# Optimization experiments

Measured on AMD Instinct MI355X. Metric: run time of the kernel, lower is better.

The kernel has to match this reference:

```python
import jax, jax.numpy as jnp
import numpy as np

B, A, H, W = 16, 3, 80, 80
NUM_CLASSES = 80
C = 4 + NUM_CLASSES  # box(4) + [obj-as-class0 + remaining classes]
N_TGT = 64


def setup_inputs() -> dict:
    key = jax.random.key(0)
    pred = jax.random.normal(key, (B, A, H, W, C), dtype=jnp.float32)
    # Build targets with DISTINCT, SORTED grid cells so that the original
    # module's boolean-mask gather order pairs cell k with target k.
    rng = np.random.default_rng(0)
    cells = np.sort(rng.choice(H * W, size=N_TGT, replace=False))
    gy, gx = cells // W, cells % W
    cls_id = rng.integers(0, NUM_CLASSES, size=N_TGT).astype(np.float32)
    wh = (rng.random((N_TGT, 2)) * 0.2 + 0.02).astype(np.float32)
    targets = np.stack(
        [cls_id, (gx + 0.5) / W, (gy + 0.5) / H, wh[:, 0], wh[:, 1]], axis=1
    ).astype(np.float32)  # [N,5] = (class, x, y, w, h)
    return {"pred": pred, "targets": jnp.asarray(targets)}


def reference(pred, targets):
    Bs, As, Hs, Ws, Cs = pred.shape
    hw = Hs * Ws
    # grid assignment: (x*W, y*H) floored and clamped, like .long().clamp_
    gx = jnp.clip(jnp.floor(targets[:, 1] * Ws), 0, Ws - 1).astype(jnp.int32)
    gy = jnp.clip(jnp.floor(targets[:, 2] * Hs), 0, Hs - 1).astype(jnp.int32)
    cells = gy * Ws + gx  # [N]

    pf = pred.reshape(Bs, As, hw, Cs)
    pc = pf[:, :, cells, :]  # gather object cells -> [B, A, N, C]

    # loc: MSE of predicted box vs target (x,y,w,h), tiled over B*A
    boxes = targets[:, 1:5]  # [N,4]
    loc_loss = jnp.mean((pc[..., :4] - boxes) ** 2)

    # cls: BCEWithLogits of pred[...,4:] vs one-hot(class) over C-4 channels
    onehot = jax.nn.one_hot(targets[:, 0].astype(jnp.int32), Cs - 4, dtype=pred.dtype)
    logits = pc[..., 4:]  # [B,A,N,C-4]
    cls_loss = jnp.mean(jax.nn.softplus(logits) - logits * onehot)

    # obj: BCEWithLogits(pred[...,4][obj_mask], 1) = softplus(-logit)
    obj_loss = jnp.mean(jax.nn.softplus(-pc[..., 4]))

    # noobj: BCEWithLogits(pred[...,4][~obj_mask], 0) = softplus(logit)
    sp = jax.nn.softplus(pf[..., 4])  # [B,A,HW]
    cell_mask = jnp.zeros(hw, pred.dtype).at[cells].set(1.0)  # unique object cells
    n_obj_cells = cell_mask.sum()
    noobj_count = Bs * As * (hw - n_obj_cells)
    noobj_loss = jnp.sum(sp * (1.0 - cell_mask)) / noobj_count

    obj_scale, noobj_scale = 1.0, 0.5
    total = loc_loss + cls_loss + obj_scale * obj_loss + noobj_scale * noobj_loss
    return total  # single prediction scale -> divide by 1
```

## Files before the change

kernel.cpp:

```cpp
#include <hip/hip_runtime.h>
#include <math.h>

constexpr int BDIM  = 256;
constexpr int Bsz   = 16, Asz = 3, Hsz = 80, Wsz = 80;
constexpr int Csz   = 84;
constexpr int HWsz  = Hsz * Wsz;
constexpr int BAsz  = Bsz * Asz;
constexpr int TOTAL = BAsz * HWsz;
constexpr int NTGT  = 64;
constexpr int NCOMBO = BAsz * NTGT;
constexpr int NBLK  = TOTAL / BDIM;

__device__ __forceinline__ float softplus_f(float x) {
    return log1pf(expf(-fabsf(x))) + fmaxf(x, 0.f);
}

__global__ __launch_bounds__(BDIM)
void yolo_main(const float* __restrict__ pred,
               const float* __restrict__ targets,
               float* __restrict__ partial) {
    int tid = blockIdx.x * BDIM + threadIdx.x;

    float sp_all = 0.f, sp_tgt = 0.f, loc = 0.f, cls = 0.f, obj = 0.f;

    {
        float p4 = pred[(size_t)tid * Csz + 4];
        sp_all = softplus_f(p4);
    }

    if (tid < NCOMBO) {
        int t  = tid & (NTGT - 1);
        int ba = tid >> 6;
        float cid_f = targets[t * 5 + 0];
        float tx    = targets[t * 5 + 1];
        float ty    = targets[t * 5 + 2];
        float tw    = targets[t * 5 + 3];
        float th    = targets[t * 5 + 4];
        int gx = min(max((int)floorf(tx * (float)Wsz), 0), Wsz - 1);
        int gy = min(max((int)floorf(ty * (float)Hsz), 0), Hsz - 1);
        int cell = gy * Wsz + gx;
        const float* p = pred + ((size_t)ba * HWsz + cell) * Csz;
        const float4* pv = (const float4*)p;

        float4 c0 = pv[0];
        float d0 = c0.x - tx, d1 = c0.y - ty, d2 = c0.z - tw, d3 = c0.w - th;
        loc = d0 * d0 + d1 * d1 + d2 * d2 + d3 * d3;

        float csum = 0.f;
        float p4 = 0.f;
        #pragma unroll
        for (int j = 1; j < 21; ++j) {
            float4 w = pv[j];
            if (j == 1) p4 = w.x;
            csum += softplus_f(w.x) + softplus_f(w.y) +
                    softplus_f(w.z) + softplus_f(w.w);
        }
        int cid = (int)cid_f;
        csum -= p[4 + cid];
        cls = csum;

        obj    = softplus_f(-p4);
        sp_tgt = softplus_f(p4);
    }

    float vals[5] = {sp_all, sp_tgt, loc, cls, obj};
    #pragma unroll
    for (int k = 0; k < 5; ++k) {
        float s = vals[k];
        #pragma unroll
        for (int o = 32; o > 0; o >>= 1) s += __shfl_down(s, o, 64);
        vals[k] = s;
    }
    __shared__ float sm[4][5];
    int lane = threadIdx.x & 63, wid = threadIdx.x >> 6;
    if (lane == 0) {
        #pragma unroll
        for (int k = 0; k < 5; ++k) sm[wid][k] = vals[k];
    }
    __syncthreads();
    if (threadIdx.x == 0) {
        #pragma unroll
        for (int k = 0; k < 5; ++k) {
            partial[blockIdx.x * 5 + k] = sm[0][k] + sm[1][k] + sm[2][k] + sm[3][k];
        }
    }
}

__global__ __launch_bounds__(BDIM)
void yolo_final(const float* __restrict__ partial, float* __restrict__ out) {
    float s[5] = {0.f, 0.f, 0.f, 0.f, 0.f};
    for (int i = threadIdx.x; i < NBLK; i += BDIM) {
        #pragma unroll
        for (int k = 0; k < 5; ++k) s[k] += partial[i * 5 + k];
    }
    #pragma unroll
    for (int k = 0; k < 5; ++k) {
        float v = s[k];
        #pragma unroll
        for (int o = 32; o > 0; o >>= 1) v += __shfl_down(v, o, 64);
        s[k] = v;
    }
    __shared__ float sm[4][5];
    int lane = threadIdx.x & 63, wid = threadIdx.x >> 6;
    if (lane == 0) {
        #pragma unroll
        for (int k = 0; k < 5; ++k) sm[wid][k] = s[k];
    }
    __syncthreads();
    if (threadIdx.x == 0) {
        float sp_all = sm[0][0] + sm[1][0] + sm[2][0] + sm[3][0];
        float sp_tgt = sm[0][1] + sm[1][1] + sm[2][1] + sm[3][1];
        float loc    = sm[0][2] + sm[1][2] + sm[2][2] + sm[3][2];
        float cls    = sm[0][3] + sm[1][3] + sm[2][3] + sm[3][3];
        float obj    = sm[0][4] + sm[1][4] + sm[2][4] + sm[3][4];
        float loc_loss = loc / (float)(NCOMBO * 4);
        float cls_loss = cls / (float)(NCOMBO * 80);
        float obj_loss = obj / (float)NCOMBO;
        float noobj    = (sp_all - sp_tgt) / (float)(BAsz * (HWsz - NTGT));
        out[0] = loc_loss + cls_loss + obj_loss + 0.5f * noobj;
    }
}

extern "C" void kernel_launch(void* const* d_in, const int* in_sizes, int n_in,
                              void* d_out, int out_size, void* d_ws, size_t ws_size,
                              hipStream_t stream) {
    const float* pred    = (const float*)d_in[0];
    const float* targets = (const float*)d_in[1];
    float* partial = (float*)d_ws;
    float* out = (float*)d_out;

    yolo_main<<<NBLK, BDIM, 0, stream>>>(pred, targets, partial);
    yolo_final<<<1, BDIM, 0, stream>>>(partial, out);
}
```

Baseline: 159.5 us.

## Split target-cell work into dedicated wave-parallel blocks and use fast softplus intrinsics

The target-cell loss work moves out of the first 12 grid blocks, where one thread handled all 84 channels of a cell serially. It now runs in 48 extra blocks, one per batch-anchor, and each wave processes one target cell per iteration with lanes spread across channels, so loads are coalesced and the softplus work is spread out. The noobj blocks now only compute and reduce a single softplus sum. Softplus switches to the __expf/__logf intrinsics, which trade some accuracy for cheaper transcendental math.

```diff
diff --git a/kernel.cpp b/kernel.cpp
--- a/kernel.cpp
+++ b/kernel.cpp
@@ -9,114 +9,128 @@
 constexpr int TOTAL = BAsz * HWsz;
 constexpr int NTGT  = 64;
 constexpr int NCOMBO = BAsz * NTGT;
-constexpr int NBLK  = TOTAL / BDIM;
+constexpr int GBLK  = TOTAL / BDIM;
+constexpr int TBLK  = BAsz;
+constexpr int NBLK  = GBLK + TBLK;
 
-__device__ __forceinline__ float softplus_f(float x) {
-    return log1pf(expf(-fabsf(x))) + fmaxf(x, 0.f);
+__device__ __forceinline__ float softplus_fast(float x) {
+    return fmaxf(x, 0.f) + __logf(1.f + __expf(-fabsf(x)));
 }
 
 __global__ __launch_bounds__(BDIM)
 void yolo_main(const float* __restrict__ pred,
                const float* __restrict__ targets,
-               float* __restrict__ partial) {
-    int tid = blockIdx.x * BDIM + threadIdx.x;
+               float* __restrict__ partial_sp,
+               float* __restrict__ partial_tgt) {
+    __shared__ float smem[NTGT * 5 + 16];
+    int lane = threadIdx.x & 63, wid = threadIdx.x >> 6;
 
-    float sp_all = 0.f, sp_tgt = 0.f, loc = 0.f, cls = 0.f, obj = 0.f;
-
-    {
-        float p4 = pred[(size_t)tid * Csz + 4];
-        sp_all = softplus_f(p4);
+    if (blockIdx.x < GBLK) {
+        int tid = blockIdx.x * BDIM + threadIdx.x;
+        float sp = softplus_fast(pred[(size_t)tid * Csz + 4]);
+        #pragma unroll
+        for (int o = 32; o > 0; o >>= 1) sp += __shfl_down(sp, o, 64);
+        if (lane == 0) smem[wid] = sp;
+        __syncthreads();
+        if (threadIdx.x == 0)
+            partial_sp[blockIdx.x] = smem[0] + smem[1] + smem[2] + smem[3];
+        return;
     }
 
-    if (tid < NCOMBO) {
-        int t  = tid & (NTGT - 1);
-        int ba = tid >> 6;
-        float cid_f = targets[t * 5 + 0];
-        float tx    = targets[t * 5 + 1];
-        float ty    = targets[t * 5 + 2];
-        float tw    = targets[t * 5 + 3];
-        float th    = targets[t * 5 + 4];
-        int gx = min(max((int)floorf(tx * (float)Wsz), 0), Wsz - 1);
-        int gy = min(max((int)floorf(ty * (float)Hsz), 0), Hsz - 1);
+    int ba = blockIdx.x - GBLK;
+    for (int i = threadIdx.x; i < NTGT * 5; i += BDIM) smem[i] = targets[i];
+    __syncthreads();
+
+    const float* __restrict__ pb = pred + (size_t)ba * HWsz * Csz;
+    float cls = 0.f, locv = 0.f, obj = 0.f, spt = 0.f;
+
+    #pragma unroll 4
+    for (int k = 0; k < NTGT / 4; ++k) {
+        int t = wid * (NTGT / 4) + k;
+        const float* tg = &smem[t * 5];
+        float cid_f = tg[0];
+        int gx = min(max((int)floorf(tg[1] * (float)Wsz), 0), Wsz - 1);
+        int gy = min(max((int)floorf(tg[2] * (float)Hsz), 0), Hsz - 1);
         int cell = gy * Wsz + gx;
-        const float* p = pred + ((size_t)ba * HWsz + cell) * Csz;
-        const float4* pv = (const float4*)p;
+        const float* p = pb + (size_t)cell * Csz;
+        int cid4 = 4 + (int)cid_f;
 
-        float4 c0 = pv[0];
-        float d0 = c0.x - tx, d1 = c0.y - ty, d2 = c0.z - tw, d3 = c0.w - th;
-        loc = d0 * d0 + d1 * d1 + d2 * d2 + d3 * d3;
-
-        float csum = 0.f;
-        float p4 = 0.f;
-        #pragma unroll
-        for (int j = 1; j < 21; ++j) {
-            float4 w = pv[j];
-            if (j == 1) p4 = w.x;
-            csum += softplus_f(w.x) + softplus_f(w.y) +
-                    softplus_f(w.z) + softplus_f(w.w);
+        float v0 = p[lane];
+        if (lane < 4) {
+            float d = v0 - tg[1 + lane];
+            locv += d * d;
+        } else {
+            cls += softplus_fast(v0);
         }
-        int cid = (int)cid_f;
-        csum -= p[4 + cid];
-        cls = csum;
-
-        obj    = softplus_f(-p4);
-        sp_tgt = softplus_f(p4);
+        if (lane == 4) {
+            obj += softplus_fast(-v0);
+            spt += softplus_fast(v0);
+        }
+        if (lane == cid4) cls -= v0;
+        if (lane < 20) {
+            float v1 = p[64 + lane];
+            cls += softplus_fast(v1);
+            if (lane + 64 == cid4) cls -= v1;
+        }
     }
 
-    float vals[5] = {sp_all, sp_tgt, loc, cls, obj};
+    float vals[4] = {cls, locv, obj, spt};
     #pragma unroll
-    for (int k = 0; k < 5; ++k) {
-        float s = vals[k];
+    for (int q = 0; q < 4; ++q) {
+        float v = vals[q];
         #pragma unroll
-        for (int o = 32; o > 0; o >>= 1) s += __shfl_down(s, o, 64);
-        vals[k] = s;
+        for (int o = 32; o > 0; o >>= 1) v += __shfl_down(v, o, 64);
+        vals[q] = v;
     }
-    __shared__ float sm[4][5];
-    int lane = threadIdx.x & 63, wid = threadIdx.x >> 6;
+    __syncthreads();
     if (lane == 0) {
         #pragma unroll
-        for (int k = 0; k < 5; ++k) sm[wid][k] = vals[k];
+        for (int q = 0; q < 4; ++q) smem[wid * 4 + q] = vals[q];
     }
     __syncthreads();
     if (threadIdx.x == 0) {
         #pragma unroll
-        for (int k = 0; k < 5; ++k) {
-            partial[blockIdx.x * 5 + k] = sm[0][k] + sm[1][k] + sm[2][k] + sm[3][k];
-        }
+        for (int q = 0; q < 4; ++q)
+            partial_tgt[ba * 4 + q] = smem[q] + smem[4 + q] + smem[8 + q] + smem[12 + q];
     }
 }
 
 __global__ __launch_bounds__(BDIM)
-void yolo_final(const float* __restrict__ partial, float* __restrict__ out) {
+void yolo_final(const float* __restrict__ partial_sp,
+                const float* __restrict__ partial_tgt,
+                float* __restrict__ out) {
+    int lane = threadIdx.x & 63, wid = threadIdx.x >> 6;
     float s[5] = {0.f, 0.f, 0.f, 0.f, 0.f};
-    for (int i = threadIdx.x; i < NBLK; i += BDIM) {
-        #pragma unroll
-        for (int k = 0; k < 5; ++k) s[k] += partial[i * 5 + k];
+    for (int i = threadIdx.x; i < GBLK; i += BDIM) s[0] += partial_sp[i];
+    if (threadIdx.x < TBLK) {
+        s[1] = partial_tgt[threadIdx.x * 4 + 0];
+        s[2] = partial_tgt[threadIdx.x * 4 + 1];
+        s[3] = partial_tgt[threadIdx.x * 4 + 2];
+        s[4] = partial_tgt[threadIdx.x * 4 + 3];
     }
     #pragma unroll
-    for (int k = 0; k < 5; ++k) {
-        float v = s[k];
+    for (int q = 0; q < 5; ++q) {
+        float v = s[q];
         #pragma unroll
         for (int o = 32; o > 0; o >>= 1) v += __shfl_down(v, o, 64);
-        s[k] = v;
+        s[q] = v;
     }
     __shared__ float sm[4][5];
-    int lane = threadIdx.x & 63, wid = threadIdx.x >> 6;
     if (lane == 0) {
         #pragma unroll
-        for (int k = 0; k < 5; ++k) sm[wid][k] = s[k];
+        for (int q = 0; q < 5; ++q) sm[wid][q] = s[q];
     }
     __syncthreads();
     if (threadIdx.x == 0) {
         float sp_all = sm[0][0] + sm[1][0] + sm[2][0] + sm[3][0];
-        float sp_tgt = sm[0][1] + sm[1][1] + sm[2][1] + sm[3][1];
+        float cls    = sm[0][1] + sm[1][1] + sm[2][1] + sm[3][1];
         float loc    = sm[0][2] + sm[1][2] + sm[2][2] + sm[3][2];
-        float cls    = sm[0][3] + sm[1][3] + sm[2][3] + sm[3][3];
-        float obj    = sm[0][4] + sm[1][4] + sm[2][4] + sm[3][4];
+        float obj    = sm[0][3] + sm[1][3] + sm[2][3] + sm[3][3];
+        float spt    = sm[0][4] + sm[1][4] + sm[2][4] + sm[3][4];
         float loc_loss = loc / (float)(NCOMBO * 4);
         float cls_loss = cls / (float)(NCOMBO * 80);
         float obj_loss = obj / (float)NCOMBO;
-        float noobj    = (sp_all - sp_tgt) / (float)(BAsz * (HWsz - NTGT));
+        float noobj    = (sp_all - spt) / (float)(BAsz * (HWsz - NTGT));
         out[0] = loc_loss + cls_loss + obj_loss + 0.5f * noobj;
     }
 }
@@ -126,9 +140,10 @@
                               hipStream_t stream) {
     const float* pred    = (const float*)d_in[0];
     const float* targets = (const float*)d_in[1];
-    float* partial = (float*)d_ws;
+    float* partial_sp  = (float*)d_ws;
+    float* partial_tgt = partial_sp + GBLK;
     float* out = (float*)d_out;
 
-    yolo_main<<<NBLK, BDIM, 0, stream>>>(pred, targets, partial);
-    yolo_final<<<1, BDIM, 0, stream>>>(partial, out);
+    yolo_main<<<NBLK, BDIM, 0, stream>>>(pred, targets, partial_sp, partial_tgt);
+    yolo_final<<<1, BDIM, 0, stream>>>(partial_sp, partial_tgt, out);
 }
```

New measurement: 155.6 us. -2.4%, faster.
